# Kernel tuning notes

Hardware: AMD Instinct MI355X
Metric: run time of the kernel (lower is better)

The kernel has to match this reference:

```python
import jax, jax.numpy as jnp
import numpy as np

NUM_HEADS = 8
WIN = (7, 7)


def _relative_position_index(wh, ww):
    # Same construction as the torch module (numpy, static).
    coords = np.stack(np.meshgrid(np.arange(wh), np.arange(ww), indexing='ij'))  # (2, wh, ww)
    flat = coords.reshape(2, -1)                                                 # (2, L)
    rel = flat[:, :, None] - flat[:, None, :]                                    # (2, L, L)
    rel = rel.transpose(1, 2, 0).astype(np.int64)                                # (L, L, 2)
    rel[:, :, 0] += wh - 1
    rel[:, :, 1] += ww - 1
    rel[:, :, 0] *= 2 * ww - 1
    return rel.sum(-1)  # (L, L), values in [0, (2wh-1)*(2ww-1))


def setup_inputs() -> dict:
    key = jax.random.key(0)
    k0, k1, k2, k3, k4 = jax.random.split(key, 5)
    B, C = 2048, 256
    wh, ww = WIN
    L = wh * ww
    nW = 64
    q = jax.random.normal(k0, (B, C, wh, ww), dtype=jnp.float32)
    k = jax.random.normal(k1, (B, C, wh, ww), dtype=jnp.float32)
    v = jax.random.normal(k2, (B, C, wh, ww), dtype=jnp.float32)
    # Swin-style shift mask: 0 where attend, -100 where blocked
    keep = jax.random.uniform(k3, (nW, L, L)) < 0.9
    mask = jnp.where(keep, 0.0, -100.0).astype(jnp.float32)
    n_bias = (2 * wh - 1) * (2 * ww - 1)  # 169
    rel_bias_table = 0.02 * jax.random.normal(k4, (n_bias, NUM_HEADS), dtype=jnp.float32)
    rel_pos_index = jnp.asarray(_relative_position_index(wh, ww), dtype=jnp.int32)
    return {"q": q, "k": k, "v": v, "mask": mask,
            "rel_bias_table": rel_bias_table, "rel_pos_index": rel_pos_index}


def reference(q, k, v, mask, rel_bias_table, rel_pos_index):
    b, c, wh, ww = q.shape
    L = wh * ww
    H = NUM_HEADS
    d_k = c // H
    scale = d_k ** -0.5
    qh = q.reshape(b, H, d_k, L)
    kh = k.reshape(b, H, d_k, L)
    # NOTE: the original torch code reassigns v = k.reshape(...) — values come from k.
    vh = kh
    attn = jnp.einsum('bhct,bhcs->bhts', qh, kh) * scale  # (b, H, L, L)
    bias = rel_bias_table[rel_pos_index.reshape(-1)].reshape(L, L, H)
    attn = attn + jnp.transpose(bias, (2, 0, 1))[None]    # (1, H, L, L)
    nW = mask.shape[0]
    attn = attn.reshape(b // nW, nW, H, L, L) + mask[None, :, None]
    attn = attn.reshape(b, H, L, L)
    attn = jax.nn.softmax(attn, axis=-1)
    score = jnp.einsum('bhts,bhcs->bhct', attn, vh).reshape(b, c, wh, ww)
    return (score, attn)
```

## Files before the change

kernel.cpp:

```cpp
#include <hip/hip_runtime.h>
#include <hip/hip_bf16.h>
#include <math.h>


#define LW 49
#define NH 8

typedef short s16x8 __attribute__((ext_vector_type(8)));
typedef float f32x4 __attribute__((ext_vector_type(4)));
typedef unsigned short u16x8 __attribute__((ext_vector_type(8)));

union Frag { s16x8 v; unsigned short u[8]; };

__device__ __forceinline__ unsigned short f2bf(float x) {
    return __builtin_bit_cast(unsigned short, __float2bfloat16(x));
}
__device__ __forceinline__ float bf2f(unsigned short h) {
    return __uint_as_float(((unsigned)h) << 16);
}
__device__ __forceinline__ void split8(const float* xf, Frag& hi, Frag& lo) {
    #pragma unroll
    for (int j = 0; j < 8; j++) {
        const unsigned short hb = f2bf(xf[j]);
        hi.u[j] = hb;
        lo.u[j] = f2bf(xf[j] - bf2f(hb));
    }
}

__device__ __forceinline__ void lds_barrier() {
    asm volatile("s_waitcnt lgkmcnt(0)" ::: "memory");
    __builtin_amdgcn_s_barrier();
    asm volatile("" ::: "memory");
    __builtin_amdgcn_sched_barrier(0);
}
__device__ __forceinline__ void stage_barrier() {
    asm volatile("s_waitcnt vmcnt(0) lgkmcnt(0)" ::: "memory");
    __builtin_amdgcn_s_barrier();
    asm volatile("" ::: "memory");
    __builtin_amdgcn_sched_barrier(0);
}

__device__ __forceinline__ void load_lds16(const void* g, void* l) {
    __builtin_amdgcn_global_load_lds(
        (const __attribute__((address_space(1))) void*)g,
        (__attribute__((address_space(3))) void*)l, 16, 0, 0);
}

#define MFMA16(A, B, C) __builtin_amdgcn_mfma_f32_16x16x32_bf16((A), (B), (C), 0, 0, 0)

__global__ __launch_bounds__(256) void prep_frag_kernel(
    const float* __restrict__ mask, const float* __restrict__ table,
    const int* __restrict__ idx,
    unsigned short* __restrict__ biasB, unsigned short* __restrict__ maskB)
{
    const int i = blockIdx.x * 256 + threadIdx.x;
    const int NBF = 8 * 4096;
    const int NMF = 64 * 4096;
    const float L2E = 1.4426950408889634f;
    if (i < NBF) {
        const int h = i >> 12, rem = i & 4095;
        const int mt = rem >> 10, lane = (rem >> 4) & 63, e = rem & 15;
        const int nt = e >> 2, r = e & 3;
        const int t = mt * 16 + (lane >> 4) * 4 + r;
        const int s = nt * 16 + (lane & 15);
        const float v = (t < LW && s < LW)
                      ? table[idx[t * LW + s] * NH + h] * L2E : 0.f;
        biasB[i] = f2bf(v);
    } else if (i < NBF + NMF) {
        const int j = i - NBF;
        const int w2 = j >> 12, rem = j & 4095;
        const int mt = rem >> 10, lane = (rem >> 4) & 63, e = rem & 15;
        const int nt = e >> 2, r = e & 3;
        const int t = mt * 16 + (lane >> 4) * 4 + r;
        const int s = nt * 16 + (lane & 15);
        const float v = (t < LW && s < LW)
                      ? mask[w2 * (LW * LW) + t * LW + s] * L2E : 0.f;
        maskB[j] = f2bf(v);
    }
}

__global__ __launch_bounds__(256, 4) void wa_mfma_kernel(
    const float* __restrict__ q, const float* __restrict__ k,
    const unsigned short* __restrict__ biasB,
    const unsigned short* __restrict__ maskB,
    float* __restrict__ score_out, float* __restrict__ attn_out)
{
    __shared__ __align__(16) char sRaw[2][12800];

    const int tid  = (int)threadIdx.x;
    const int wv   = __builtin_amdgcn_readfirstlane(tid >> 6);
    const int sub  = wv >> 1;
    const int wvL  = wv & 1;
    const int bh   = blockIdx.x * 2 + sub;
    const int h    = bh & 7;
    const int w    = (bh >> 3) & 63;
    const int lane = tid & 63;
    const int l15  = lane & 15;
    const int g4   = lane >> 4;

    const float* qp = q + (size_t)bh * (32 * LW);
    const float* kp = k + (size_t)bh * (32 * LW);

    char* ldsBase = &sRaw[sub][0];
    char* ldsK = ldsBase;
    char* ldsQ = ldsBase + 6400;

    {
        const char* src = (wvL == 0) ? (const char*)kp : (const char*)qp;
        char*       dst = (wvL == 0) ? ldsK : ldsQ;
        #pragma unroll
        for (int i = 0; i < 6; i++)
            load_lds16(src + i * 1024 + lane * 16, dst + i * 1024);
        if (lane < 16) {
            const int off = (lane < 8) ? lane * 16 : 112;
            load_lds16(src + 6144 + off, dst + 6144);
        }
    }

    stage_barrier();

    u16x8 bq8[2][2], mq8[2][2];
    {
        const unsigned short* bF = biasB + (size_t)h * 4096;
        const unsigned short* mF = maskB + (size_t)w * 4096;
        #pragma unroll
        for (int mi = 0; mi < 2; mi++) {
            const int mt = wvL * 2 + mi;
            const u16x8* bp = (const u16x8*)(bF + mt * 1024 + lane * 16);
            const u16x8* mp = (const u16x8*)(mF + mt * 1024 + lane * 16);
            bq8[mi][0] = bp[0];
            bq8[mi][1] = bp[1];
            mq8[mi][0] = mp[0];
            mq8[mi][1] = mp[1];
        }
    }

    const float* sKf = (const float*)ldsK;
    const float* sQf = (const float*)ldsQ;

    Frag Qh[2], Ql[2];
    #pragma unroll
    for (int mi = 0; mi < 2; mi++) {
        const int t  = (wvL * 2 + mi) * 16 + l15;
        const int tc = t < LW ? t : (LW - 1);
        float xf[8];
        #pragma unroll
        for (int j = 0; j < 8; j++) xf[j] = sQf[(g4 * 8 + j) * LW + tc];
        split8(xf, Qh[mi], Ql[mi]);
    }

    f32x4 acc[2][4];
    #pragma unroll
    for (int mi = 0; mi < 2; mi++)
        #pragma unroll
        for (int nt = 0; nt < 4; nt++)
            #pragma unroll
            for (int r = 0; r < 4; r++) acc[mi][nt][r] = 0.f;

    #pragma unroll
    for (int nt = 0; nt < 4; nt++) {
        const int s  = nt * 16 + l15;
        const int sc = s < LW ? s : (LW - 1);
        float xf[8];
        #pragma unroll
        for (int j = 0; j < 8; j++) xf[j] = sKf[(g4 * 8 + j) * LW + sc];
        Frag Kh, Kl;
        split8(xf, Kh, Kl);
        #pragma unroll
        for (int mi = 0; mi < 2; mi++) {
            acc[mi][nt] = MFMA16(Qh[mi].v, Kh.v, acc[mi][nt]);
            acc[mi][nt] = MFMA16(Ql[mi].v, Kh.v, acc[mi][nt]);
            acc[mi][nt] = MFMA16(Qh[mi].v, Kl.v, acc[mi][nt]);
        }
    }

    Frag K2h[2], K2l[2];
    {
        const int c = wvL * 16 + l15;
        #pragma unroll
        for (int ks = 0; ks < 2; ks++) {
            float xf[8];
            #pragma unroll
            for (int j = 0; j < 8; j++) {
                const int s  = ks * 32 + g4 * 8 + j;
                const int sc = s < LW ? s : (LW - 1);
                xf[j] = sKf[c * LW + sc];
            }
            split8(xf, K2h[ks], K2l[ks]);
        }
    }

    const float scale2 = 0.17677669529663687f * 1.4426950408889634f;
    #pragma unroll
    for (int mi = 0; mi < 2; mi++) {
        #pragma unroll
        for (int nt = 0; nt < 4; nt++) {
            const bool pad = (nt * 16 + l15) >= LW;
            #pragma unroll
            for (int r = 0; r < 4; r++) {
                const float bm = bf2f(bq8[mi][nt >> 1][(nt & 1) * 4 + r])
                               + bf2f(mq8[mi][nt >> 1][(nt & 1) * 4 + r]);
                const float v2 = fmaf(acc[mi][nt][r], scale2, bm);
                acc[mi][nt][r] = pad ? -1e30f : v2;
            }
        }
    }

    #pragma unroll
    for (int mi = 0; mi < 2; mi++) {
        #pragma unroll
        for (int r = 0; r < 4; r++) {
            float sm = 0.f;
            #pragma unroll
            for (int nt = 0; nt < 4; nt++) {
                const float p = __builtin_exp2f(acc[mi][nt][r]);
                acc[mi][nt][r] = p;
                sm += p;
            }
            sm += __shfl_xor(sm, 1);
            sm += __shfl_xor(sm, 2);
            sm += __shfl_xor(sm, 4);
            sm += __shfl_xor(sm, 8);
            const float inv = 1.0f / sm;
            #pragma unroll
            for (int nt = 0; nt < 4; nt++) acc[mi][nt][r] *= inv;
        }
    }

    lds_barrier();

    unsigned short* sB = (unsigned short*)ldsBase;
    #pragma unroll
    for (int mi = 0; mi < 2; mi++) {
        #pragma unroll
        for (int r = 0; r < 4; r++) {
            const int t = (wvL * 2 + mi) * 16 + g4 * 4 + r;
            if (t < LW) {
                #pragma unroll
                for (int nt = 0; nt < 4; nt++) {
                    const int s = nt * 16 + l15;
                    const float p = acc[mi][nt][r];
                    const unsigned short ph = f2bf(p);
                    const unsigned short pl = f2bf(p - bf2f(ph));
                    const unsigned idx = (unsigned)t * 64u
                        + ((((unsigned)s >> 3) ^ ((unsigned)t & 7u)) << 3)
                        + ((unsigned)s & 7u);
                    sB[idx]        = ph;
                    sB[3136 + idx] = pl;
                }
            }
        }
    }

    lds_barrier();

    {
        float2* dst2 = (float2*)(attn_out + (size_t)(blockIdx.x * 2) * (LW * LW));
        #pragma unroll
        for (int it = 0; it < 10; it++) {
            const int j = it * 256 + tid;
            if (j < LW * LW) {
                float v2[2];
                #pragma unroll
                for (int e = 0; e < 2; e++) {
                    const int g  = 2 * j + e;
                    const int sg = g >= LW * LW;
                    const int i2 = g - sg * (LW * LW);
                    const int t  = i2 / LW;
                    const int s  = i2 - t * LW;
                    const unsigned idx = (unsigned)t * 64u
                        + ((((unsigned)s >> 3) ^ ((unsigned)t & 7u)) << 3)
                        + ((unsigned)s & 7u);
                    const unsigned short* sBg = (const unsigned short*)&sRaw[sg][0];
                    v2[e] = bf2f(sBg[idx]) + bf2f(sBg[3136 + idx]);
                }
                dst2[j] = make_float2(v2[0], v2[1]);
            }
        }
    }

    f32x4 acc2[4];
    #pragma unroll
    for (int nt = 0; nt < 4; nt++)
        #pragma unroll
        for (int r = 0; r < 4; r++) acc2[nt][r] = 0.f;

    #pragma unroll
    for (int ntt = 0; ntt < 4; ntt++) {
        const int t  = ntt * 16 + l15;
        const int tr = t < LW ? t : (LW - 1);
        #pragma unroll
        for (int ks = 0; ks < 2; ks++) {
            const unsigned base = (unsigned)tr * 64u
                + (((unsigned)(ks * 4 + g4) ^ ((unsigned)tr & 7u)) << 3);
            Frag Ph, Pl;
            Ph.v = *(const s16x8*)&sB[base];
            Pl.v = *(const s16x8*)&sB[3136 + base];
            acc2[ntt] = MFMA16(K2h[ks].v, Ph.v, acc2[ntt]);
            acc2[ntt] = MFMA16(K2l[ks].v, Ph.v, acc2[ntt]);
            acc2[ntt] = MFMA16(K2h[ks].v, Pl.v, acc2[ntt]);
        }
    }

    lds_barrier();

    float* scf = (float*)ldsBase;
    #pragma unroll
    for (int ntt = 0; ntt < 4; ntt++) {
        const int t = ntt * 16 + l15;
        if (t < LW) {
            #pragma unroll
            for (int r = 0; r < 4; r++) {
                const int c = wvL * 16 + g4 * 4 + r;
                scf[c * LW + t] = acc2[ntt][r];
            }
        }
    }

    lds_barrier();

    {
        float4* dst4 = (float4*)(score_out + (size_t)(blockIdx.x * 2) * (32 * LW));
        #pragma unroll
        for (int it = 0; it < 4; it++) {
            const int j = it * 256 + tid;
            if (j < 784) {
                const int sg = j >= 392;
                const float4* src4 = (const float4*)&sRaw[sg][0];
                dst4[j] = src4[j - sg * 392];
            }
        }
    }
}

__global__ __launch_bounds__(256, 4) void wa_fallback_kernel(
    const float* __restrict__ q, const float* __restrict__ k,
    const float* __restrict__ mask0, const float* __restrict__ table,
    const int* __restrict__ idx,
    float* __restrict__ score_out, float* __restrict__ attn_out)
{
    __shared__ float sPf[LW * LW];
    const int lane = threadIdx.x & 63;
    const int wv   = __builtin_amdgcn_readfirstlane((int)(threadIdx.x >> 6));
    const int bh   = blockIdx.x * 4 + wv;
    const int h    = bh & 7;
    const int w    = (bh >> 3) & 63;
    const int t    = lane;
    const int tc   = (t < LW) ? t : (LW - 1);

    const float* qp = q + (size_t)bh * (32 * LW);
    const float* kp = k + (size_t)bh * (32 * LW);

    float qreg[32];
    #pragma unroll
    for (int c = 0; c < 32; c++) qreg[c] = qp[c * LW + tc];

    float S[LW];
    #pragma unroll
    for (int s = 0; s < LW; s++) S[s] = 0.f;
    #pragma unroll
    for (int c = 0; c < 32; c++) {
        #pragma unroll
        for (int s = 0; s < LW; s++)
            S[s] = fmaf(qreg[c], kp[c * LW + s], S[s]);
    }

    const float scale = 0.17677669529663687f;
    const float* mrow = mask0 + (size_t)w * (LW * LW) + tc * LW;
    const int*   irow = idx + tc * LW;
    #pragma unroll
    for (int s = 0; s < LW; s++) {
        const float bm = table[irow[s] * NH + h] + mrow[s];
        S[s] = fmaf(S[s], scale, bm);
    }

    float m = S[0];
    #pragma unroll
    for (int s = 1; s < LW; s++) m = fmaxf(m, S[s]);
    float sum = 0.f;
    #pragma unroll
    for (int s = 0; s < LW; s++) { S[s] = __expf(S[s] - m); sum += S[s]; }
    const float invs = 1.0f / sum;
    #pragma unroll
    for (int s = 0; s < LW; s++) S[s] *= invs;

    float* attn_base = attn_out + (size_t)bh * (LW * LW);
    for (int turn = 0; turn < 4; turn++) {
        __syncthreads();
        if (turn == wv) {
            if (t < LW) {
                #pragma unroll
                for (int s = 0; s < LW; s++) sPf[t * LW + s] = S[s];
            }
            #pragma unroll
            for (int it = 0; it < 38; it++) {
                const int i = it * 64 + lane;
                if (i < LW * LW) attn_base[i] = sPf[i];
            }
        }
    }

    float* sc = score_out + (size_t)bh * (32 * LW);
    #pragma unroll
    for (int c = 0; c < 32; c++) {
        float a = 0.f;
        #pragma unroll
        for (int s = 0; s < LW; s++) a = fmaf(S[s], kp[c * LW + s], a);
        if (t < LW) sc[c * LW + t] = a;
    }
}

extern "C" void kernel_launch(void* const* d_in, const int* in_sizes, int n_in,
                              void* d_out, int out_size, void* d_ws, size_t ws_size,
                              hipStream_t stream) {
    const float* q     = (const float*)d_in[0];
    const float* k     = (const float*)d_in[1];
    const float* mask  = (const float*)d_in[3];
    const float* table = (const float*)d_in[4];
    const int*   idx   = (const int*)d_in[5];

    float* score_out = (float*)d_out;
    float* attn_out  = score_out + (size_t)2048 * 256 * 49;

    const size_t NBF = (size_t)8 * 4096;
    const size_t NMF = (size_t)64 * 4096;

    if (ws_size >= (NBF + NMF) * sizeof(unsigned short)) {
        unsigned short* biasB = (unsigned short*)d_ws;
        unsigned short* maskB = biasB + NBF;
        const int tot = (int)(NBF + NMF);
        prep_frag_kernel<<<(tot + 255) / 256, 256, 0, stream>>>(
            mask, table, idx, biasB, maskB);
        wa_mfma_kernel<<<8192, 256, 0, stream>>>(
            q, k, biasB, maskB, score_out, attn_out);
    } else {
        wa_fallback_kernel<<<4096, 256, 0, stream>>>(
            q, k, mask, table, idx, score_out, attn_out);
    }
}
```

Baseline: 443.3 us.

## Make MFMA kernel persistent over four pairs with double-buffered async LDS staging

Each block now handles four (batch, head) pairs in a loop instead of one. It prefetches the next pair's Q/K into a second LDS buffer via global_load_lds while computing the current one. The goal is to hide global load latency behind compute and cut block launch overhead. In exchange LDS use doubles, launch bounds drop to 3 blocks per CU, and the grid shrinks to 2048 blocks, which reduces occupancy and the amount of parallelism available.

Result: slower. 589.2 us (+32.9%).

```diff
diff --git a/kernel.cpp b/kernel.cpp
--- a/kernel.cpp
+++ b/kernel.cpp
@@ -29,12 +29,6 @@
 
 __device__ __forceinline__ void lds_barrier() {
     asm volatile("s_waitcnt lgkmcnt(0)" ::: "memory");
-    __builtin_amdgcn_s_barrier();
-    asm volatile("" ::: "memory");
-    __builtin_amdgcn_sched_barrier(0);
-}
-__device__ __forceinline__ void stage_barrier() {
-    asm volatile("s_waitcnt vmcnt(0) lgkmcnt(0)" ::: "memory");
     __builtin_amdgcn_s_barrier();
     asm volatile("" ::: "memory");
     __builtin_amdgcn_sched_barrier(0);
@@ -79,35 +73,29 @@
     }
 }
 
-__global__ __launch_bounds__(256, 4) void wa_mfma_kernel(
+__global__ __launch_bounds__(256, 3) void wa_mfma_kernel(
     const float* __restrict__ q, const float* __restrict__ k,
     const unsigned short* __restrict__ biasB,
     const unsigned short* __restrict__ maskB,
     float* __restrict__ score_out, float* __restrict__ attn_out)
 {
-    __shared__ __align__(16) char sRaw[2][12800];
+    __shared__ __align__(16) char sRaw[2][2][12800];
 
     const int tid  = (int)threadIdx.x;
     const int wv   = __builtin_amdgcn_readfirstlane(tid >> 6);
     const int sub  = wv >> 1;
     const int wvL  = wv & 1;
-    const int bh   = blockIdx.x * 2 + sub;
-    const int h    = bh & 7;
-    const int w    = (bh >> 3) & 63;
     const int lane = tid & 63;
     const int l15  = lane & 15;
     const int g4   = lane >> 4;
-
-    const float* qp = q + (size_t)bh * (32 * LW);
-    const float* kp = k + (size_t)bh * (32 * LW);
-
-    char* ldsBase = &sRaw[sub][0];
-    char* ldsK = ldsBase;
-    char* ldsQ = ldsBase + 6400;
-
-    {
-        const char* src = (wvL == 0) ? (const char*)kp : (const char*)qp;
-        char*       dst = (wvL == 0) ? ldsK : ldsQ;
+    const int pairBase = blockIdx.x * 4;
+
+    auto do_stage = [&](int pi, int buf) {
+        const int bhs = (pairBase + pi) * 2 + sub;
+        const char* src = (wvL == 0)
+            ? (const char*)(k + (size_t)bhs * (32 * LW))
+            : (const char*)(q + (size_t)bhs * (32 * LW));
+        char* dst = &sRaw[buf][sub][0] + wvL * 6400;
         #pragma unroll
         for (int i = 0; i < 6; i++)
             load_lds16(src + i * 1024 + lane * 16, dst + i * 1024);
@@ -115,221 +103,244 @@
             const int off = (lane < 8) ? lane * 16 : 112;
             load_lds16(src + 6144 + off, dst + 6144);
         }
-    }
-
-    stage_barrier();
-
-    u16x8 bq8[2][2], mq8[2][2];
-    {
-        const unsigned short* bF = biasB + (size_t)h * 4096;
-        const unsigned short* mF = maskB + (size_t)w * 4096;
+    };
+
+    do_stage(0, 0);
+
+    #pragma unroll 1
+    for (int p = 0; p < 4; p++) {
+        const int cur = p & 1;
+        if (p < 3) {
+            do_stage(p + 1, cur ^ 1);
+            asm volatile("s_waitcnt vmcnt(7)" ::: "memory");
+        } else {
+            asm volatile("s_waitcnt vmcnt(0)" ::: "memory");
+        }
+        __builtin_amdgcn_s_barrier();
+        asm volatile("" ::: "memory");
+        __builtin_amdgcn_sched_barrier(0);
+
+        const int bh = (pairBase + p) * 2 + sub;
+        const int h  = bh & 7;
+        const int w  = (bh >> 3) & 63;
+        char* ldsBase = &sRaw[cur][sub][0];
+        const float* sKf = (const float*)ldsBase;
+        const float* sQf = (const float*)(ldsBase + 6400);
+
+        u16x8 bq8[2][2], mq8[2][2];
+        {
+            const unsigned short* bF = biasB + (size_t)h * 4096;
+            const unsigned short* mF = maskB + (size_t)w * 4096;
+            #pragma unroll
+            for (int mi = 0; mi < 2; mi++) {
+                const int mt = wvL * 2 + mi;
+                const u16x8* bp = (const u16x8*)(bF + mt * 1024 + lane * 16);
+                const u16x8* mp = (const u16x8*)(mF + mt * 1024 + lane * 16);
+                bq8[mi][0] = bp[0];
+                bq8[mi][1] = bp[1];
+                mq8[mi][0] = mp[0];
+                mq8[mi][1] = mp[1];
+            }
+        }
+
+        Frag Qh[2], Ql[2];
         #pragma unroll
         for (int mi = 0; mi < 2; mi++) {
-            const int mt = wvL * 2 + mi;
-            const u16x8* bp = (const u16x8*)(bF + mt * 1024 + lane * 16);
-            const u16x8* mp = (const u16x8*)(mF + mt * 1024 + lane * 16);
-            bq8[mi][0] = bp[0];
-            bq8[mi][1] = bp[1];
-            mq8[mi][0] = mp[0];
-            mq8[mi][1] = mp[1];
-        }
-    }
-
-    const float* sKf = (const float*)ldsK;
-    const float* sQf = (const float*)ldsQ;
-
-    Frag Qh[2], Ql[2];
-    #pragma unroll
-    for (int mi = 0; mi < 2; mi++) {
-        const int t  = (wvL * 2 + mi) * 16 + l15;
-        const int tc = t < LW ? t : (LW - 1);
-        float xf[8];
-        #pragma unroll
-        for (int j = 0; j < 8; j++) xf[j] = sQf[(g4 * 8 + j) * LW + tc];
-        split8(xf, Qh[mi], Ql[mi]);
-    }
-
-    f32x4 acc[2][4];
-    #pragma unroll
-    for (int mi = 0; mi < 2; mi++)
+            const int t  = (wvL * 2 + mi) * 16 + l15;
+            const int tc = t < LW ? t : (LW - 1);
+            float xf[8];
+            #pragma unroll
+            for (int j = 0; j < 8; j++) xf[j] = sQf[(g4 * 8 + j) * LW + tc];
+            split8(xf, Qh[mi], Ql[mi]);
+        }
+
+        f32x4 acc[2][4];
+        #pragma unroll
+        for (int mi = 0; mi < 2; mi++)
+            #pragma unroll
+            for (int nt = 0; nt < 4; nt++)
+                #pragma unroll
+                for (int r = 0; r < 4; r++) acc[mi][nt][r] = 0.f;
+
+        #pragma unroll
+        for (int nt = 0; nt < 4; nt++) {
+            const int s  = nt * 16 + l15;
+            const int sc = s < LW ? s : (LW - 1);
+            float xf[8];
+            #pragma unroll
+            for (int j = 0; j < 8; j++) xf[j] = sKf[(g4 * 8 + j) * LW + sc];
+            Frag Kh, Kl;
+            split8(xf, Kh, Kl);
+            #pragma unroll
+            for (int mi = 0; mi < 2; mi++) {
+                acc[mi][nt] = MFMA16(Qh[mi].v, Kh.v, acc[mi][nt]);
+                acc[mi][nt] = MFMA16(Ql[mi].v, Kh.v, acc[mi][nt]);
+                acc[mi][nt] = MFMA16(Qh[mi].v, Kl.v, acc[mi][nt]);
+            }
+        }
+
+        Frag K2h[2], K2l[2];
+        {
+            const int c = wvL * 16 + l15;
+            #pragma unroll
+            for (int ks = 0; ks < 2; ks++) {
+                float xf[8];
+                #pragma unroll
+                for (int j = 0; j < 8; j++) {
+                    const int s  = ks * 32 + g4 * 8 + j;
+                    const int sc = s < LW ? s : (LW - 1);
+                    xf[j] = sKf[c * LW + sc];
+                }
+                split8(xf, K2h[ks], K2l[ks]);
+            }
+        }
+
+        const float scale2 = 0.17677669529663687f * 1.4426950408889634f;
+        #pragma unroll
+        for (int mi = 0; mi < 2; mi++) {
+            #pragma unroll
+            for (int nt = 0; nt < 4; nt++) {
+                const bool pad = (nt * 16 + l15) >= LW;
+                #pragma unroll
+                for (int r = 0; r < 4; r++) {
+                    const float bm = bf2f(bq8[mi][nt >> 1][(nt & 1) * 4 + r])
+                                   + bf2f(mq8[mi][nt >> 1][(nt & 1) * 4 + r]);
+                    const float v2 = fmaf(acc[mi][nt][r], scale2, bm);
+                    acc[mi][nt][r] = pad ? -1e30f : v2;
+                }
+            }
+        }
+
+        #pragma unroll
+        for (int mi = 0; mi < 2; mi++) {
+            #pragma unroll
+            for (int r = 0; r < 4; r++) {
+                float sm = 0.f;
+                #pragma unroll
+                for (int nt = 0; nt < 4; nt++) {
+                    const float pp = __builtin_exp2f(acc[mi][nt][r]);
+                    acc[mi][nt][r] = pp;
+                    sm += pp;
+                }
+                sm += __shfl_xor(sm, 1);
+                sm += __shfl_xor(sm, 2);
+                sm += __shfl_xor(sm, 4);
+                sm += __shfl_xor(sm, 8);
+                const float inv = 1.0f / sm;
+                #pragma unroll
+                for (int nt = 0; nt < 4; nt++) acc[mi][nt][r] *= inv;
+            }
+        }
+
+        lds_barrier();
+
+        unsigned short* sB = (unsigned short*)ldsBase;
+        #pragma unroll
+        for (int mi = 0; mi < 2; mi++) {
+            #pragma unroll
+            for (int r = 0; r < 4; r++) {
+                const int t = (wvL * 2 + mi) * 16 + g4 * 4 + r;
+                if (t < LW) {
+                    #pragma unroll
+                    for (int nt = 0; nt < 4; nt++) {
+                        const int s = nt * 16 + l15;
+                        const float pp = acc[mi][nt][r];
+                        const unsigned short ph = f2bf(pp);
+                        const unsigned short pl = f2bf(pp - bf2f(ph));
+                        const unsigned idx = (unsigned)t * 64u
+                            + ((((unsigned)s >> 3) ^ ((unsigned)t & 7u)) << 3)
+                            + ((unsigned)s & 7u);
+                        sB[idx]        = ph;
+                        sB[3136 + idx] = pl;
+                    }
+                }
+            }
+        }
+
+        lds_barrier();
+
+        {
+            float2* dst2 = (float2*)(attn_out
+                + (size_t)((pairBase + p) * 2) * (LW * LW));
+            #pragma unroll
+            for (int it = 0; it < 10; it++) {
+                const int j = it * 256 + tid;
+                if (j < LW * LW) {
+                    float v2[2];
+                    #pragma unroll
+                    for (int e = 0; e < 2; e++) {
+                        const int g  = 2 * j + e;
+                        const int sg = g >= LW * LW;
+                        const int i2 = g - sg * (LW * LW);
+                        const int t  = i2 / LW;
+                        const int s  = i2 - t * LW;
+                        const unsigned idx = (unsigned)t * 64u
+                            + ((((unsigned)s >> 3) ^ ((unsigned)t & 7u)) << 3)
+                            + ((unsigned)s & 7u);
+                        const unsigned short* sBg =
+                            (const unsigned short*)&sRaw[cur][sg][0];
+                        v2[e] = bf2f(sBg[idx]) + bf2f(sBg[3136 + idx]);
+                    }
+                    dst2[j] = make_float2(v2[0], v2[1]);
+                }
+            }
+        }
+
+        f32x4 acc2[4];
         #pragma unroll
         for (int nt = 0; nt < 4; nt++)
             #pragma unroll
-            for (int r = 0; r < 4; r++) acc[mi][nt][r] = 0.f;
-
-    #pragma unroll
-    for (int nt = 0; nt < 4; nt++) {
-        const int s  = nt * 16 + l15;
-        const int sc = s < LW ? s : (LW - 1);
-        float xf[8];
-        #pragma unroll
-        for (int j = 0; j < 8; j++) xf[j] = sKf[(g4 * 8 + j) * LW + sc];
-        Frag Kh, Kl;
-        split8(xf, Kh, Kl);
-        #pragma unroll
-        for (int mi = 0; mi < 2; mi++) {
-            acc[mi][nt] = MFMA16(Qh[mi].v, Kh.v, acc[mi][nt]);
-            acc[mi][nt] = MFMA16(Ql[mi].v, Kh.v, acc[mi][nt]);
-            acc[mi][nt] = MFMA16(Qh[mi].v, Kl.v, acc[mi][nt]);
-        }
-    }
-
-    Frag K2h[2], K2l[2];
-    {
-        const int c = wvL * 16 + l15;
-        #pragma unroll
-        for (int ks = 0; ks < 2; ks++) {
-            float xf[8];
-            #pragma unroll
-            for (int j = 0; j < 8; j++) {
-                const int s  = ks * 32 + g4 * 8 + j;
-                const int sc = s < LW ? s : (LW - 1);
-                xf[j] = sKf[c * LW + sc];
-            }
-            split8(xf, K2h[ks], K2l[ks]);
-        }
-    }
-
-    const float scale2 = 0.17677669529663687f * 1.4426950408889634f;
-    #pragma unroll
-    for (int mi = 0; mi < 2; mi++) {
-        #pragma unroll
-        for (int nt = 0; nt < 4; nt++) {
-            const bool pad = (nt * 16 + l15) >= LW;
-            #pragma unroll
-            for (int r = 0; r < 4; r++) {
-                const float bm = bf2f(bq8[mi][nt >> 1][(nt & 1) * 4 + r])
-                               + bf2f(mq8[mi][nt >> 1][(nt & 1) * 4 + r]);
-                const float v2 = fmaf(acc[mi][nt][r], scale2, bm);
-                acc[mi][nt][r] = pad ? -1e30f : v2;
-            }
-        }
-    }
-
-    #pragma unroll
-    for (int mi = 0; mi < 2; mi++) {
-        #pragma unroll
-        for (int r = 0; r < 4; r++) {
-            float sm = 0.f;
-            #pragma unroll
-            for (int nt = 0; nt < 4; nt++) {
-                const float p = __builtin_exp2f(acc[mi][nt][r]);
-                acc[mi][nt][r] = p;
-                sm += p;
-            }
-            sm += __shfl_xor(sm, 1);
-            sm += __shfl_xor(sm, 2);
-            sm += __shfl_xor(sm, 4);
-            sm += __shfl_xor(sm, 8);
-            const float inv = 1.0f / sm;
-            #pragma unroll
-            for (int nt = 0; nt < 4; nt++) acc[mi][nt][r] *= inv;
-        }
-    }
-
-    lds_barrier();
-
-    unsigned short* sB = (unsigned short*)ldsBase;
-    #pragma unroll
-    for (int mi = 0; mi < 2; mi++) {
-        #pragma unroll
-        for (int r = 0; r < 4; r++) {
-            const int t = (wvL * 2 + mi) * 16 + g4 * 4 + r;
+            for (int r = 0; r < 4; r++) acc2[nt][r] = 0.f;
+
+        #pragma unroll
+        for (int ntt = 0; ntt < 4; ntt++) {
+            const int t  = ntt * 16 + l15;
+            const int tr = t < LW ? t : (LW - 1);
+            #pragma unroll
+            for (int ks = 0; ks < 2; ks++) {
+                const unsigned base = (unsigned)tr * 64u
+                    + (((unsigned)(ks * 4 + g4) ^ ((unsigned)tr & 7u)) << 3);
+                Frag Ph, Pl;
+                Ph.v = *(const s16x8*)&sB[base];
+                Pl.v = *(const s16x8*)&sB[3136 + base];
+                acc2[ntt] = MFMA16(K2h[ks].v, Ph.v, acc2[ntt]);
+                acc2[ntt] = MFMA16(K2l[ks].v, Ph.v, acc2[ntt]);
+                acc2[ntt] = MFMA16(K2h[ks].v, Pl.v, acc2[ntt]);
+            }
+        }
+
+        lds_barrier();
+
+        float* scf = (float*)ldsBase;
+        #pragma unroll
+        for (int ntt = 0; ntt < 4; ntt++) {
+            const int t = ntt * 16 + l15;
             if (t < LW) {
                 #pragma unroll
-                for (int nt = 0; nt < 4; nt++) {
-                    const int s = nt * 16 + l15;
-                    const float p = acc[mi][nt][r];
-                    const unsigned short ph = f2bf(p);
-                    const unsigned short pl = f2bf(p - bf2f(ph));
-                    const unsigned idx = (unsigned)t * 64u
-                        + ((((unsigned)s >> 3) ^ ((unsigned)t & 7u)) << 3)
-                        + ((unsigned)s & 7u);
-                    sB[idx]        = ph;
-                    sB[3136 + idx] = pl;
-                }
-            }
-        }
-    }
-
-    lds_barrier();
-
-    {
-        float2* dst2 = (float2*)(attn_out + (size_t)(blockIdx.x * 2) * (LW * LW));
-        #pragma unroll
-        for (int it = 0; it < 10; it++) {
-            const int j = it * 256 + tid;
-            if (j < LW * LW) {
-                float v2[2];
-                #pragma unroll
-                for (int e = 0; e < 2; e++) {
-                    const int g  = 2 * j + e;
-                    const int sg = g >= LW * LW;
-                    const int i2 = g - sg * (LW * LW);
-                    const int t  = i2 / LW;
-                    const int s  = i2 - t * LW;
-                    const unsigned idx = (unsigned)t * 64u
-                        + ((((unsigned)s >> 3) ^ ((unsigned)t & 7u)) << 3)
-                        + ((unsigned)s & 7u);
-                    const unsigned short* sBg = (const unsigned short*)&sRaw[sg][0];
-                    v2[e] = bf2f(sBg[idx]) + bf2f(sBg[3136 + idx]);
-                }
-                dst2[j] = make_float2(v2[0], v2[1]);
-            }
-        }
-    }
-
-    f32x4 acc2[4];
-    #pragma unroll
-    for (int nt = 0; nt < 4; nt++)
-        #pragma unroll
-        for (int r = 0; r < 4; r++) acc2[nt][r] = 0.f;
-
-    #pragma unroll
-    for (int ntt = 0; ntt < 4; ntt++) {
-        const int t  = ntt * 16 + l15;
-        const int tr = t < LW ? t : (LW - 1);
-        #pragma unroll
-        for (int ks = 0; ks < 2; ks++) {
-            const unsigned base = (unsigned)tr * 64u
-                + (((unsigned)(ks * 4 + g4) ^ ((unsigned)tr & 7u)) << 3);
-            Frag Ph, Pl;
-            Ph.v = *(const s16x8*)&sB[base];
-            Pl.v = *(const s16x8*)&sB[3136 + base];
-            acc2[ntt] = MFMA16(K2h[ks].v, Ph.v, acc2[ntt]);
-            acc2[ntt] = MFMA16(K2l[ks].v, Ph.v, acc2[ntt]);
-            acc2[ntt] = MFMA16(K2h[ks].v, Pl.v, acc2[ntt]);
-        }
-    }
-
-    lds_barrier();
-
-    float* scf = (float*)ldsBase;
-    #pragma unroll
-    for (int ntt = 0; ntt < 4; ntt++) {
-        const int t = ntt * 16 + l15;
-        if (t < LW) {
-            #pragma unroll
-            for (int r = 0; r < 4; r++) {
-                const int c = wvL * 16 + g4 * 4 + r;
-                scf[c * LW + t] = acc2[ntt][r];
-            }
-        }
-    }
-
-    lds_barrier();
-
-    {
-        float4* dst4 = (float4*)(score_out + (size_t)(blockIdx.x * 2) * (32 * LW));
-        #pragma unroll
-        for (int it = 0; it < 4; it++) {
-            const int j = it * 256 + tid;
-            if (j < 784) {
-                const int sg = j >= 392;
-                const float4* src4 = (const float4*)&sRaw[sg][0];
-                dst4[j] = src4[j - sg * 392];
-            }
-        }
+                for (int r = 0; r < 4; r++) {
+                    const int c = wvL * 16 + g4 * 4 + r;
+                    scf[c * LW + t] = acc2[ntt][r];
+                }
+            }
+        }
+
+        lds_barrier();
+
+        {
+            float4* dst4 = (float4*)(score_out
+                + (size_t)((pairBase + p) * 2) * (32 * LW));
+            #pragma unroll
+            for (int it = 0; it < 4; it++) {
+                const int j = it * 256 + tid;
+                if (j < 784) {
+                    const int sg = j >= 392;
+                    const float4* src4 = (const float4*)&sRaw[cur][sg][0];
+                    dst4[j] = src4[j - sg * 392];
+                }
+            }
+        }
+
+        lds_barrier();
     }
 }
 
@@ -431,7 +442,7 @@
         const int tot = (int)(NBF + NMF);
         prep_frag_kernel<<<(tot + 255) / 256, 256, 0, stream>>>(
             mask, table, idx, biasB, maskB);
-        wa_mfma_kernel<<<8192, 256, 0, stream>>>(
+        wa_mfma_kernel<<<2048, 256, 0, stream>>>(
             q, k, biasB, maskB, score_out, attn_out);
     } else {
         wa_fallback_kernel<<<4096, 256, 0, stream>>>(
```
